# Kernel tuning notes

Measured on AMD Instinct MI355X. Metric: run time of the kernel, lower is better.

Reference implementation:

```python
import jax, jax.numpy as jnp
import numpy as np

B, T, I, H, L = 32, 1024, 1024, 1024, 3


def setup_inputs() -> dict:
    key = jax.random.key(0)
    ks = jax.random.split(key, 8)
    sc_in = 1.0 / np.sqrt(I)
    sc_h = 1.0 / np.sqrt(H)
    return {
        "x": jax.random.normal(ks[0], (B, T, I), dtype=jnp.float32),
        "s0": jnp.zeros((B, H), dtype=jnp.float32),
        "w_h": jax.random.normal(ks[1], (I, H), dtype=jnp.float32) * sc_in,
        "w_t": jax.random.normal(ks[2], (I, H), dtype=jnp.float32) * sc_in,
        "w_c": jax.random.normal(ks[3], (I, H), dtype=jnp.float32) * sc_in,
        "Rh": jax.random.normal(ks[4], (L, H, H), dtype=jnp.float32) * sc_h,
        "Rt": jax.random.normal(ks[5], (L, H, H), dtype=jnp.float32) * sc_h,
        "Rc": jax.random.normal(ks[6], (L, H, H), dtype=jnp.float32) * sc_h,
        "bh": jnp.zeros((L, H), dtype=jnp.float32),
        "bt": jnp.zeros((L, H), dtype=jnp.float32),
        "bc": jnp.zeros((L, H), dtype=jnp.float32),
    }


def reference(x, s0, w_h, w_t, w_c, Rh, Rt, Rc, bh, bt, bc):
    # x: [B, T, I]; s0: [B, H]. Dropout prob = 0 -> identity.
    num_layers = Rh.shape[0]

    def step(s, x_t):
        # Input projections only feed layer 0 (as in the torch code).
        whx = x_t @ w_h  # [B, H]
        wtx = x_t @ w_t
        wcx = x_t @ w_c
        for l in range(num_layers):
            h_in = (whx if l == 0 else 0.0) + s @ Rh[l].T + bh[l]
            t_in = (wtx if l == 0 else 0.0) + s @ Rt[l].T + bt[l]
            c_in = (wcx if l == 0 else 0.0) + s @ Rc[l].T + bc[l]
            h = jnp.tanh(h_in)
            t = jax.nn.sigmoid(t_in)
            c = jax.nn.sigmoid(c_in)
            s = h * t + s * c
        return s, s

    x_tbi = jnp.swapaxes(x, 0, 1)  # [T, B, I] for scan over time
    s_T, outs = jax.lax.scan(step, s0, x_tbi)
    return jnp.swapaxes(outs, 0, 1), s_T  # ([B, T, H], [B, H])
```

## Files before the change

kernel.cpp:

```cpp
#include <hip/hip_runtime.h>
#include <hip/hip_bf16.h>

static constexpr int Bb = 32;
static constexpr int Tt = 1024;
static constexpr int Ii = 1024;
static constexpr int Hh = 1024;
static constexpr int NWG = 256;

static constexpr int SLOT_E = Hh * Bb;
static constexpr int NS     = 16;

typedef float f4 __attribute__((ext_vector_type(4)));

static constexpr int LDS_WORDS = 36 * 1024 + 2 * 1536;
static constexpr int LDS_BYTES = LDS_WORDS * 4;

template <typename PT> __device__ __forceinline__ float pt_to_f(PT v);
template <> __device__ __forceinline__ float pt_to_f<float>(float v) { return v; }
template <> __device__ __forceinline__ float pt_to_f<__hip_bfloat16>(__hip_bfloat16 v) { return __bfloat162float(v); }

template <typename PT> __device__ __forceinline__ PT f_to_pt(float v);
template <> __device__ __forceinline__ float f_to_pt<float>(float v) { return v; }
template <> __device__ __forceinline__ __hip_bfloat16 f_to_pt<__hip_bfloat16>(float v) { return __float2bfloat16(v); }

__device__ __forceinline__ void backoff(int it) {
    if (it < 2)      __builtin_amdgcn_s_sleep(1);
    else if (it < 4) __builtin_amdgcn_s_sleep(2);
    else if (it < 8) __builtin_amdgcn_s_sleep(4);
    else             __builtin_amdgcn_s_sleep(8);
}

#define BGLD(dst, p, lit) \
    asm volatile("global_load_dwordx4 %0, %1, off offset:" lit " sc0 sc1" : "=v"(dst) : "v"(p))
#define BG8(sv, p, a,b,c,d2,e,f,g2,h) \
    BGLD(sv[0],p,a); BGLD(sv[1],p,b); BGLD(sv[2],p,c); BGLD(sv[3],p,d2); \
    BGLD(sv[4],p,e); BGLD(sv[5],p,f); BGLD(sv[6],p,g2); BGLD(sv[7],p,h)
#define VWAIT(n) do { asm volatile("s_waitcnt vmcnt(" #n ")" ::: "memory"); \
                      __builtin_amdgcn_sched_barrier(0); } while (0)

__device__ __forceinline__ int grp_tag32(const f4* sv, unsigned texp) {
    int ok = 1;
#pragma unroll
    for (int i = 0; i < 8; ++i)
#pragma unroll
        for (int j = 0; j < 4; ++j)
            ok &= (int)((__float_as_uint(sv[i][j]) & 3u) == texp);
    return ok;
}

#define RETRY32T(sv, texp, p, a,b,c,d2,e,f,g2,h) \
    { int _it = 0; \
      while (!__all(grp_tag32(sv, texp))) { \
          if (_it) backoff(_it); \
          ++_it; \
          BG8(sv, p, a,b,c,d2,e,f,g2,h); \
          VWAIT(0); \
      } }

template <typename PT>
__global__ __launch_bounds__(256, 2) void proj_gemm(
    const float* __restrict__ X, const float* __restrict__ Wh,
    const float* __restrict__ Wt, const float* __restrict__ Wc,
    PT* __restrict__ P2)
{
    __shared__ float smem[4160];
    float* As = smem;
    float* Bs = smem + 1088;

    const int tid = threadIdx.x;
    const int tx = tid & 15, ty = tid >> 4;
    const int col0 = blockIdx.x * 64;
    const int t0 = blockIdx.y * 2;

    float acc[3][4][4];
#pragma unroll
    for (int g = 0; g < 3; ++g)
#pragma unroll
        for (int mm = 0; mm < 4; ++mm)
#pragma unroll
            for (int nn = 0; nn < 4; ++nn) acc[g][mm][nn] = 0.f;

    const int lm = tid >> 2, lk4 = (tid & 3) * 4;
    const float* aptr = X + ((size_t)(lm & 31) * Tt + (t0 + (lm >> 5))) * Ii + lk4;
    const int bk = tid >> 4, bn4 = (tid & 15) * 4;

    for (int k0 = 0; k0 < Ii; k0 += 16) {
        float4 av = *(const float4*)(aptr + k0);
        As[(lk4 + 0) * 68 + lm] = av.x;
        As[(lk4 + 1) * 68 + lm] = av.y;
        As[(lk4 + 2) * 68 + lm] = av.z;
        As[(lk4 + 3) * 68 + lm] = av.w;
        *(float4*)&Bs[0 * 1024 + bk * 64 + bn4] = *(const float4*)(Wh + (size_t)(k0 + bk) * Hh + col0 + bn4);
        *(float4*)&Bs[1 * 1024 + bk * 64 + bn4] = *(const float4*)(Wt + (size_t)(k0 + bk) * Hh + col0 + bn4);
        *(float4*)&Bs[2 * 1024 + bk * 64 + bn4] = *(const float4*)(Wc + (size_t)(k0 + bk) * Hh + col0 + bn4);
        __syncthreads();
#pragma unroll
        for (int k = 0; k < 16; ++k) {
            float4 a = *(const float4*)&As[k * 68 + ty * 4];
            float a_[4] = {a.x, a.y, a.z, a.w};
#pragma unroll
            for (int g = 0; g < 3; ++g) {
                float4 b = *(const float4*)&Bs[g * 1024 + k * 64 + tx * 4];
                float b_[4] = {b.x, b.y, b.z, b.w};
#pragma unroll
                for (int mm = 0; mm < 4; ++mm)
#pragma unroll
                    for (int nn = 0; nn < 4; ++nn)
                        acc[g][mm][nn] += a_[mm] * b_[nn];
            }
        }
        __syncthreads();
    }

    float* E = smem;
    const int b4 = (tid & 7) * 4;
#pragma unroll 1
    for (int g = 0; g < 3; ++g) {
        __syncthreads();
#pragma unroll
        for (int mm = 0; mm < 4; ++mm)
#pragma unroll
            for (int nn = 0; nn < 4; ++nn)
                E[(ty * 4 + mm) * 65 + tx * 4 + nn] = acc[g][mm][nn];
        __syncthreads();
        PT* dst = P2 + (size_t)g * Tt * Hh * Bb;
#pragma unroll
        for (int it = 0; it < 4; ++it) {
            const int line = (tid >> 3) + it * 32;
            const int tt = line >> 6, hh = line & 63;
            const float o0 = E[(tt * 32 + b4 + 0) * 65 + hh];
            const float o1 = E[(tt * 32 + b4 + 1) * 65 + hh];
            const float o2v = E[(tt * 32 + b4 + 2) * 65 + hh];
            const float o3 = E[(tt * 32 + b4 + 3) * 65 + hh];
            PT* d = dst + ((size_t)(t0 + tt) * Hh + col0 + hh) * Bb + b4;
            d[0] = f_to_pt<PT>(o0); d[1] = f_to_pt<PT>(o1);
            d[2] = f_to_pt<PT>(o2v); d[3] = f_to_pt<PT>(o3);
        }
    }
}

__global__ __launch_bounds__(256) void init_ring_s(const float* __restrict__ s0,
                                                   float* __restrict__ ring)
{
    const size_t tid = (size_t)blockIdx.x * 256 + threadIdx.x;
    if (tid < (size_t)Bb * Hh) {
        const int b = (int)(tid >> 10), h = (int)(tid & 1023);
        ring[h * 32 + b] = __uint_as_float(__float_as_uint(s0[tid]) & ~3u);
    }
    const uint4 pat = {3u, 3u, 3u, 3u};
    uint4* base = (uint4*)(ring + SLOT_E);
    const size_t n16 = (size_t)(NS - 1) * SLOT_E * 4 / 16;
    const size_t stride = (size_t)gridDim.x * 256;
    for (size_t i = tid; i < n16; i += stride) base[i] = pat;
}

__global__ __launch_bounds__(256) void out_transpose_hist(
    const float* __restrict__ shist, float* __restrict__ out, float* __restrict__ sT)
{
    __shared__ float tile[128 * 33];
    const int tid = threadIdx.x;
    const int h0 = blockIdx.x * 128;
    const int t = blockIdx.y;
    const float* src = shist + ((size_t)t * Hh + h0) * Bb;
#pragma unroll
    for (int e = 0; e < 16; ++e) {
        const int idx = e * 256 + tid;
        tile[(idx >> 5) * 33 + (idx & 31)] = src[idx];
    }
    __syncthreads();
    const int hi = tid & 31, bq = tid >> 5;
#pragma unroll
    for (int e = 0; e < 4; ++e) {
        const int b = bq + e * 8;
        float4 v;
        v.x = tile[(hi * 4 + 0) * 33 + b];
        v.y = tile[(hi * 4 + 1) * 33 + b];
        v.z = tile[(hi * 4 + 2) * 33 + b];
        v.w = tile[(hi * 4 + 3) * 33 + b];
        *(float4*)(out + ((size_t)b * Tt + t) * Hh + h0 + hi * 4) = v;
        if (t == Tt - 1) *(float4*)(sT + (size_t)b * Hh + h0 + hi * 4) = v;
    }
}

template <typename PT>
__global__ __launch_bounds__(256, 1) void rhn_recur(
    const float* __restrict__ Rh, const float* __restrict__ Rt,
    const float* __restrict__ Rc, const float* __restrict__ bh,
    const float* __restrict__ bt, const float* __restrict__ bc,
    const PT* __restrict__ P2, float* __restrict__ ring,
    float* __restrict__ shist, const float* __restrict__ s0in)
{
    extern __shared__ float lds[];

    const int g = blockIdx.x;
    const int tid = threadIdx.x;

    {
        const int k4 = tid * 4;
        const int sk = k4 ^ (((k4 >> 5) & 7) << 2);
#pragma unroll 1
        for (int j = 0; j < 36; ++j) {
            const int l = j / 12;
            const int rem = j - l * 12;
            const int gt = rem >> 2;
            const int q = rem & 3;
            const int h = (q << 8) | g;
            const float* src = (gt == 0 ? Rh : (gt == 1 ? Rt : Rc)) + ((size_t)l * Hh + h) * Hh;
            *(float4*)&lds[(j << 10) | sk] = *(const float4*)(src + k4);
        }
    }
    __syncthreads();

    const int ks = tid >> 3;
    const int b0 = (tid & 7) << 2;
    const int q8 = ks & 7;
    const int wv = tid >> 6;
    const int ub = tid & 31;
    const int uqc = (tid >> 5) & 3;
    const int uhc = (uqc << 8) | g;

    int o2[8];
#pragma unroll
    for (int c = 0; c < 8; ++c) o2[c] = ((c ^ q8) << 2);

    float brh[3], brt[3], brc[3];
#pragma unroll
    for (int l = 0; l < 3; ++l) {
        brh[l] = bh[l * Hh + uhc];
        brt[l] = bt[l * Hh + uhc];
        brc[l] = bc[l * Hh + uhc];
    }

    float so_reg = (tid < 128) ? s0in[(size_t)ub * Hh + uhc] : 0.f;

#pragma unroll 1
    for (int t = 0; t < Tt; ++t) {
#pragma unroll 1
        for (int l = 0; l < 3; ++l) {
            const int p = t * 3 + l;
            const int slr = p & (NS - 1);
            const unsigned texp = (unsigned)((p >> 4) & 3);
            const int slw = (p + 1) & (NS - 1);
            const unsigned twr = (unsigned)(((p + 1) >> 4) & 3);
            float* part = lds + 36 * 1024 + (p & 1) * 1536;

            float pv0 = 0.f, pv1 = 0.f, pv2 = 0.f;
            if (l == 0 && tid < 128) {
                const size_t pb = ((size_t)t * Hh + uhc) * Bb + ub;
                pv0 = pt_to_f<PT>(P2[pb]);
                pv1 = pt_to_f<PT>(P2[(size_t)Tt * Hh * Bb + pb]);
                pv2 = pt_to_f<PT>(P2[2 * (size_t)Tt * Hh * Bb + pb]);
            }

            const float* rp = lds + l * 12288 + (ks << 5);

            f4 accv[12];
#pragma unroll
            for (int jj = 0; jj < 12; ++jj) accv[jj] = (f4){0.f, 0.f, 0.f, 0.f};

            const float* sA = ring + (size_t)slr * SLOT_E + (ks << 5) * 32 + b0;
            f4 sv0[8], sv1[8];
            BG8(sv0, sA, "0","128","256","384","512","640","768","896");
            BG8(sv1, sA, "1024","1152","1280","1408","1536","1664","1792","1920");
            VWAIT(8);
            RETRY32T(sv0, texp, sA, "0","128","256","384","512","640","768","896");
#pragma unroll
            for (int jj = 0; jj < 12; ++jj) {
                const f4 r0 = *(const f4*)(rp + jj * 1024 + o2[0]);
                const f4 r1 = *(const f4*)(rp + jj * 1024 + o2[1]);
                f4 a = accv[jj];
                a += sv0[0] * r0[0]; a += sv0[1] * r0[1]; a += sv0[2] * r0[2]; a += sv0[3] * r0[3];
                a += sv0[4] * r1[0]; a += sv0[5] * r1[1]; a += sv0[6] * r1[2]; a += sv0[7] * r1[3];
                accv[jj] = a;
            }
            BG8(sv0, sA, "2048","2176","2304","2432","2560","2688","2816","2944");
            VWAIT(8);
            RETRY32T(sv1, texp, sA, "1024","1152","1280","1408","1536","1664","1792","1920");
#pragma unroll
            for (int jj = 0; jj < 12; ++jj) {
                const f4 r0 = *(const f4*)(rp + jj * 1024 + o2[2]);
                const f4 r1 = *(const f4*)(rp + jj * 1024 + o2[3]);
                f4 a = accv[jj];
                a += sv1[0] * r0[0]; a += sv1[1] * r0[1]; a += sv1[2] * r0[2]; a += sv1[3] * r0[3];
                a += sv1[4] * r1[0]; a += sv1[5] * r1[1]; a += sv1[6] * r1[2]; a += sv1[7] * r1[3];
                accv[jj] = a;
            }
            BG8(sv1, sA, "3072","3200","3328","3456","3584","3712","3840","3968");
            VWAIT(8);
            RETRY32T(sv0, texp, sA, "2048","2176","2304","2432","2560","2688","2816","2944");
#pragma unroll
            for (int jj = 0; jj < 12; ++jj) {
                const f4 r0 = *(const f4*)(rp + jj * 1024 + o2[4]);
                const f4 r1 = *(const f4*)(rp + jj * 1024 + o2[5]);
                f4 a = accv[jj];
                a += sv0[0] * r0[0]; a += sv0[1] * r0[1]; a += sv0[2] * r0[2]; a += sv0[3] * r0[3];
                a += sv0[4] * r1[0]; a += sv0[5] * r1[1]; a += sv0[6] * r1[2]; a += sv0[7] * r1[3];
                accv[jj] = a;
            }
            VWAIT(0);
            RETRY32T(sv1, texp, sA, "3072","3200","3328","3456","3584","3712","3840","3968");
#pragma unroll
            for (int jj = 0; jj < 12; ++jj) {
                const f4 r0 = *(const f4*)(rp + jj * 1024 + o2[6]);
                const f4 r1 = *(const f4*)(rp + jj * 1024 + o2[7]);
                f4 a = accv[jj];
                a += sv1[0] * r0[0]; a += sv1[1] * r0[1]; a += sv1[2] * r0[2]; a += sv1[3] * r0[3];
                a += sv1[4] * r1[0]; a += sv1[5] * r1[1]; a += sv1[6] * r1[2]; a += sv1[7] * r1[3];
                accv[jj] = a;
            }

#pragma unroll
            for (int jj = 0; jj < 12; ++jj) {
#pragma unroll
                for (int st = 8; st <= 32; st <<= 1) {
                    accv[jj][0] += __shfl_xor(accv[jj][0], st);
                    accv[jj][1] += __shfl_xor(accv[jj][1], st);
                    accv[jj][2] += __shfl_xor(accv[jj][2], st);
                    accv[jj][3] += __shfl_xor(accv[jj][3], st);
                }
            }
            f4 s1 = accv[0];
#pragma unroll
            for (int j2 = 1; j2 < 8; ++j2) if (q8 == j2) s1 = accv[j2];
            f4 s2 = accv[8];
#pragma unroll
            for (int j2 = 1; j2 < 4; ++j2) if (q8 == j2) s2 = accv[8 + j2];
            *(f4*)&part[(wv * 12 + q8) * 32 + b0] = s1;
            if (q8 < 4) *(f4*)&part[(wv * 12 + 8 + q8) * 32 + b0] = s2;
            __syncthreads();

            if (tid < 128) {
                float vals[3];
#pragma unroll
                for (int gt = 0; gt < 3; ++gt) {
                    const int jl = (gt << 2) + uqc;
                    vals[gt] = part[jl * 32 + ub] + part[(12 + jl) * 32 + ub]
                             + part[(24 + jl) * 32 + ub] + part[(36 + jl) * 32 + ub];
                }
                float bb0, bb1, bb2;
                if (l == 0)      { bb0 = brh[0]; bb1 = brt[0]; bb2 = brc[0]; }
                else if (l == 1) { bb0 = brh[1]; bb1 = brt[1]; bb2 = brc[1]; }
                else             { bb0 = brh[2]; bb1 = brt[2]; bb2 = brc[2]; }
                vals[0] += bb0; vals[1] += bb1; vals[2] += bb2;
                if (l == 0) { vals[0] += pv0; vals[1] += pv1; vals[2] += pv2; }
                const float hv = 1.f - 2.f / (1.f + __expf(2.f * vals[0]));
                const float tv = 1.f / (1.f + __expf(-vals[1]));
                const float cv = 1.f / (1.f + __expf(-vals[2]));
                const float sn = hv * tv + so_reg * cv;
                so_reg = sn;
                const unsigned bits = (__float_as_uint(sn) & ~3u) | twr;
                __hip_atomic_store((unsigned*)(ring + (size_t)slw * SLOT_E + uhc * 32 + ub),
                                   bits, __ATOMIC_RELAXED, __HIP_MEMORY_SCOPE_AGENT);
                if (l == 2)
                    shist[((size_t)t * Hh + uhc) * Bb + ub] = sn;
            }
        }
    }
}

template <typename PT>
static void launch_recur(const float* Rh, const float* Rt, const float* Rc,
                         const float* bh, const float* bt, const float* bc,
                         const PT* P2, float* ring, float* shist,
                         const float* s0, hipStream_t stream)
{
    (void)hipFuncSetAttribute(reinterpret_cast<const void*>(rhn_recur<PT>),
                              hipFuncAttributeMaxDynamicSharedMemorySize, LDS_BYTES);
    void* args[] = {(void*)&Rh, (void*)&Rt, (void*)&Rc, (void*)&bh, (void*)&bt, (void*)&bc,
                    (void*)&P2, (void*)&ring, (void*)&shist, (void*)&s0};
    hipError_t e = hipLaunchCooperativeKernel(reinterpret_cast<void*>(rhn_recur<PT>),
                                              dim3(NWG), dim3(256), args, LDS_BYTES, stream);
    if (e != hipSuccess) {
        rhn_recur<PT><<<dim3(NWG), dim3(256), LDS_BYTES, stream>>>(
            Rh, Rt, Rc, bh, bt, bc, P2, ring, shist, s0);
    }
}

extern "C" void kernel_launch(void* const* d_in, const int* in_sizes, int n_in,
                              void* d_out, int out_size, void* d_ws, size_t ws_size,
                              hipStream_t stream)
{
    (void)in_sizes; (void)n_in; (void)out_size;
    const float* x  = (const float*)d_in[0];
    const float* s0 = (const float*)d_in[1];
    const float* wh = (const float*)d_in[2];
    const float* wt = (const float*)d_in[3];
    const float* wc = (const float*)d_in[4];
    const float* Rh = (const float*)d_in[5];
    const float* Rt = (const float*)d_in[6];
    const float* Rc = (const float*)d_in[7];
    const float* bh = (const float*)d_in[8];
    const float* bt = (const float*)d_in[9];
    const float* bc = (const float*)d_in[10];

    float* out = (float*)d_out;
    float* sT  = out + (size_t)Bb * Tt * Hh;

    const size_t THB   = (size_t)Tt * Hh * Bb;
    const size_t p2f   = 3 * THB * 4, p2h = 3 * THB * 2;
    const size_t ringS = (size_t)NS * SLOT_E * 4;
    const size_t shF   = THB * 4;

    char* w = (char*)d_ws;

    if (ws_size >= p2f + ringS + shF + 4096) {
        float* P2 = (float*)w;
        float* ring = (float*)(w + p2f);
        float* shist = (float*)(w + p2f + ringS);
        proj_gemm<float><<<dim3(16, 512), 256, 0, stream>>>(x, wh, wt, wc, P2);
        init_ring_s<<<128, 256, 0, stream>>>(s0, ring);
        launch_recur<float>(Rh, Rt, Rc, bh, bt, bc, P2, ring, shist, s0, stream);
        out_transpose_hist<<<dim3(8, 1024), 256, 0, stream>>>(shist, out, sT);
    } else {
        __hip_bfloat16* P2 = (__hip_bfloat16*)w;
        float* ring = (float*)(w + p2h);
        float* shist = (float*)(w + p2h + ringS);
        proj_gemm<__hip_bfloat16><<<dim3(16, 512), 256, 0, stream>>>(x, wh, wt, wc, P2);
        init_ring_s<<<128, 256, 0, stream>>>(s0, ring);
        launch_recur<__hip_bfloat16>(Rh, Rt, Rc, bh, bt, bc, P2, ring, shist, s0, stream);
        out_transpose_hist<<<dim3(8, 1024), 256, 0, stream>>>(shist, out, sT);
    }
}
```

Measured before the change: 32.54 ms.

## Remap threads so each wave owns batch slice, removing LDS partial reduction barrier

Reassigns the thread-to-work mapping in the recurrent kernel. Each wavefront now covers all K-slices for its own 8 batch columns, so the full dot-product reduction completes inside the wave with xor-shuffles. This removes the LDS partial-sum buffer and the per-step __syncthreads, both on the serial critical path of every layer step. In exchange there are more shuffle stages per step, ring reads of 4-float chunks strided by 1024 instead of the previous pattern, and a different output lane layout for the state write.

```diff
diff --git a/kernel.cpp b/kernel.cpp
--- a/kernel.cpp
+++ b/kernel.cpp
@@ -12,7 +12,7 @@
 
 typedef float f4 __attribute__((ext_vector_type(4)));
 
-static constexpr int LDS_WORDS = 36 * 1024 + 2 * 1536;
+static constexpr int LDS_WORDS = 36 * 1024;
 static constexpr int LDS_BYTES = LDS_WORDS * 4;
 
 template <typename PT> __device__ __forceinline__ float pt_to_f(PT v);
@@ -211,27 +211,33 @@
     }
     __syncthreads();
 
-    const int ks = tid >> 3;
-    const int b0 = (tid & 7) << 2;
-    const int q8 = ks & 7;
-    const int wv = tid >> 6;
-    const int ub = tid & 31;
-    const int uqc = (tid >> 5) & 3;
-    const int uhc = (uqc << 8) | g;
+    const int w    = tid >> 6;
+    const int lane = tid & 63;
+    const int ksp  = lane >> 1;
+    const int bq   = lane & 1;
+    const int q8   = ksp & 7;
+    const int bb   = w * 8 + bq * 4;
+
+    const int oq  = (lane >> 1) & 3;
+    const int obe = lane >> 3;
+    const int ob  = w * 8 + (lane & 1) * 4 + obe;
+    const int oh  = (oq << 8) | g;
 
     int o2[8];
 #pragma unroll
     for (int c = 0; c < 8; ++c) o2[c] = ((c ^ q8) << 2);
 
     float brh[3], brt[3], brc[3];
-#pragma unroll
-    for (int l = 0; l < 3; ++l) {
-        brh[l] = bh[l * Hh + uhc];
-        brt[l] = bt[l * Hh + uhc];
-        brc[l] = bc[l * Hh + uhc];
-    }
-
-    float so_reg = (tid < 128) ? s0in[(size_t)ub * Hh + uhc] : 0.f;
+    if (lane < 32) {
+#pragma unroll
+        for (int l = 0; l < 3; ++l) {
+            brh[l] = bh[l * Hh + oh];
+            brt[l] = bt[l * Hh + oh];
+            brc[l] = bc[l * Hh + oh];
+        }
+    }
+
+    float so_reg = (lane < 32) ? s0in[(size_t)ob * Hh + oh] : 0.f;
 
 #pragma unroll 1
     for (int t = 0; t < Tt; ++t) {
@@ -242,23 +248,22 @@
             const unsigned texp = (unsigned)((p >> 4) & 3);
             const int slw = (p + 1) & (NS - 1);
             const unsigned twr = (unsigned)(((p + 1) >> 4) & 3);
-            float* part = lds + 36 * 1024 + (p & 1) * 1536;
 
             float pv0 = 0.f, pv1 = 0.f, pv2 = 0.f;
-            if (l == 0 && tid < 128) {
-                const size_t pb = ((size_t)t * Hh + uhc) * Bb + ub;
+            if (l == 0 && lane < 32) {
+                const size_t pb = ((size_t)t * Hh + oh) * Bb + ob;
                 pv0 = pt_to_f<PT>(P2[pb]);
                 pv1 = pt_to_f<PT>(P2[(size_t)Tt * Hh * Bb + pb]);
                 pv2 = pt_to_f<PT>(P2[2 * (size_t)Tt * Hh * Bb + pb]);
             }
 
-            const float* rp = lds + l * 12288 + (ks << 5);
+            const float* rp = lds + l * 12288 + (ksp << 5);
+            const float* sA = ring + (size_t)slr * SLOT_E + (size_t)ksp * 1024 + bb;
 
             f4 accv[12];
 #pragma unroll
             for (int jj = 0; jj < 12; ++jj) accv[jj] = (f4){0.f, 0.f, 0.f, 0.f};
 
-            const float* sA = ring + (size_t)slr * SLOT_E + (ks << 5) * 32 + b0;
             f4 sv0[8], sv1[8];
             BG8(sv0, sA, "0","128","256","384","512","640","768","896");
             BG8(sv1, sA, "1024","1152","1280","1408","1536","1664","1792","1920");
@@ -312,30 +317,22 @@
 #pragma unroll
             for (int jj = 0; jj < 12; ++jj) {
 #pragma unroll
-                for (int st = 8; st <= 32; st <<= 1) {
+                for (int st = 2; st <= 32; st <<= 1) {
                     accv[jj][0] += __shfl_xor(accv[jj][0], st);
                     accv[jj][1] += __shfl_xor(accv[jj][1], st);
                     accv[jj][2] += __shfl_xor(accv[jj][2], st);
                     accv[jj][3] += __shfl_xor(accv[jj][3], st);
                 }
             }
-            f4 s1 = accv[0];
-#pragma unroll
-            for (int j2 = 1; j2 < 8; ++j2) if (q8 == j2) s1 = accv[j2];
-            f4 s2 = accv[8];
-#pragma unroll
-            for (int j2 = 1; j2 < 4; ++j2) if (q8 == j2) s2 = accv[8 + j2];
-            *(f4*)&part[(wv * 12 + q8) * 32 + b0] = s1;
-            if (q8 < 4) *(f4*)&part[(wv * 12 + 8 + q8) * 32 + b0] = s2;
-            __syncthreads();
-
-            if (tid < 128) {
+
+            if (lane < 32) {
                 float vals[3];
 #pragma unroll
                 for (int gt = 0; gt < 3; ++gt) {
-                    const int jl = (gt << 2) + uqc;
-                    vals[gt] = part[jl * 32 + ub] + part[(12 + jl) * 32 + ub]
-                             + part[(24 + jl) * 32 + ub] + part[(36 + jl) * 32 + ub];
+                    const f4 v = accv[gt * 4 + oq];
+                    const float e01 = (obe & 1) ? v[1] : v[0];
+                    const float e23 = (obe & 1) ? v[3] : v[2];
+                    vals[gt] = (obe & 2) ? e23 : e01;
                 }
                 float bb0, bb1, bb2;
                 if (l == 0)      { bb0 = brh[0]; bb1 = brt[0]; bb2 = brc[0]; }
@@ -349,10 +346,10 @@
                 const float sn = hv * tv + so_reg * cv;
                 so_reg = sn;
                 const unsigned bits = (__float_as_uint(sn) & ~3u) | twr;
-                __hip_atomic_store((unsigned*)(ring + (size_t)slw * SLOT_E + uhc * 32 + ub),
+                __hip_atomic_store((unsigned*)(ring + (size_t)slw * SLOT_E + oh * 32 + ob),
                                    bits, __ATOMIC_RELAXED, __HIP_MEMORY_SCOPE_AGENT);
                 if (l == 2)
-                    shist[((size_t)t * Hh + uhc) * Bb + ub] = sn;
+                    shist[((size_t)t * Hh + oh) * Bb + ob] = sn;
             }
         }
     }
```

Measured after the change: 70.35 ms. +116.2%, slower.
